# Optimization experiments

Hardware: AMD Instinct MI355X
Metric: run time of the kernel (lower is better)

Reference implementation:

```python
import jax, jax.numpy as jnp
import numpy as np

N = 50000   # nodes in both graphs
E = 800000  # edges per graph
IN = 128
OUT = 64
NEG_SLOPE = 0.2  # DGL GATConv default


def setup_inputs() -> dict:
    key = jax.random.key(0)
    ks = jax.random.split(key, 12)
    stdv = 1.0 / np.sqrt(OUT)
    return {
        'h': jax.random.normal(ks[0], (N, IN), dtype=jnp.float32),
        'src0': jax.random.randint(ks[1], (E,), 0, N, dtype=jnp.int32),
        'dst0': jax.random.randint(ks[2], (E,), 0, N, dtype=jnp.int32),
        'row2': jax.random.randint(ks[3], (E,), 0, N, dtype=jnp.int32),
        'col2': jax.random.randint(ks[4], (E,), 0, N, dtype=jnp.int32),
        'adj_val': jax.random.uniform(ks[5], (E,), dtype=jnp.float32),
        # GATConv params (1 head)
        'W_gat': jax.random.normal(ks[6], (IN, OUT), dtype=jnp.float32) * 0.1,
        'attn_l': jax.random.normal(ks[7], (OUT,), dtype=jnp.float32) * 0.1,
        'attn_r': jax.random.normal(ks[8], (OUT,), dtype=jnp.float32) * 0.1,
        'bias_gat': jnp.zeros((OUT,), dtype=jnp.float32),
        # GraphConvolution params
        'W_gc': jax.random.uniform(ks[9], (IN, OUT), minval=-stdv, maxval=stdv, dtype=jnp.float32),
        'bias_gc': jax.random.uniform(ks[10], (OUT,), minval=-stdv, maxval=stdv, dtype=jnp.float32),
    }


def reference(h, src0, dst0, row2, col2, adj_val, W_gat, attn_l, attn_r, bias_gat, W_gc, bias_gc):
    n = h.shape[0]
    # ---- branch 0: GATConv(1 head) + elu activation ----
    feat = h @ W_gat                        # [N, OUT]
    el = feat @ attn_l                      # [N]
    er = feat @ attn_r                      # [N]
    e = el[src0] + er[dst0]                 # [E]
    e = jnp.where(e > 0, e, NEG_SLOPE * e)  # leaky_relu
    # edge softmax over incoming edges of each dst (stable)
    m = jax.ops.segment_max(e, dst0, num_segments=n)
    ex = jnp.exp(e - m[dst0])
    s = jax.ops.segment_sum(ex, dst0, num_segments=n)
    alpha = ex / s[dst0]                    # [E]
    agg = jax.ops.segment_sum(alpha[:, None] * feat[src0], dst0, num_segments=n)
    z1 = jax.nn.elu(agg + bias_gat)         # [N, OUT]
    # ---- branch 1: GraphConvolution: elu(adj @ (h @ W) + b) ----
    support = h @ W_gc                      # [N, OUT]
    gc = jax.ops.segment_sum(adj_val[:, None] * support[col2], row2, num_segments=n)
    z2 = jax.nn.elu(gc + bias_gc)           # [N, OUT]
    # ---- semantic attention tail (forward is just split+concat) ----
    return jnp.concatenate((z1, z2), axis=1)  # [N, 2*OUT]
```

## Files before the change

kernel.cpp:

```cpp
#include <hip/hip_runtime.h>
#include <hip/hip_bf16.h>
#include <math.h>

#define IN_F 128
#define OUT_F 64
#define BKT_SH 8
#define BKT_MASK 255
#define CHUNK 4096
#define MAXTB 800
#define IDX_BITS 24
#define IDX_MASK ((1u << IDX_BITS) - 1u)
#define PAD 16

typedef __attribute__((ext_vector_type(8))) short bf16x8;
typedef __attribute__((ext_vector_type(4))) float f32x4;

__device__ inline short f2bf(float x) {
    __hip_bfloat16 b = __float2bfloat16(x);
    return *reinterpret_cast<short*>(&b);
}
__device__ inline float bflo(unsigned u) { return __uint_as_float(u << 16); }
__device__ inline float bfhi(unsigned u) { return __uint_as_float(u & 0xffff0000u); }

__global__ __launch_bounds__(256) void k_fused(const float* __restrict__ h,
                                               const float* __restrict__ Wg,
                                               const float* __restrict__ Wc,
                                               const float* __restrict__ attn_l,
                                               const float* __restrict__ attn_r,
                                               __hip_bfloat16* __restrict__ feat,
                                               __hip_bfloat16* __restrict__ support,
                                               float* __restrict__ el,
                                               float* __restrict__ er, int n, int G1,
                                               const int* __restrict__ dst0,
                                               const int* __restrict__ row2,
                                               int* __restrict__ bcnt,
                                               int* __restrict__ chunkhist,
                                               int NB, int E_) {
    __shared__ short Wl[16][128][8];
    __shared__ int hist[MAXTB];

    if ((int)blockIdx.x >= G1) {
        int TB = 2 * NB;
        int t = threadIdx.x;
        int chunk = (int)blockIdx.x - G1;
        for (int i = t; i < TB; i += 256) hist[i] = 0;
        __syncthreads();
        int e0 = chunk * CHUNK;
        for (int i = t; i < CHUNK; i += 256) {
            int e = e0 + i;
            if (e < E_) {
                atomicAdd(&hist[dst0[e] >> BKT_SH], 1);
                atomicAdd(&hist[NB + (row2[e] >> BKT_SH)], 1);
            }
        }
        __syncthreads();
        int* hrow = chunkhist + (size_t)chunk * TB;
        for (int b = t; b < TB; b += 256) {
            int c = hist[b];
            hrow[b] = c;
            if (c) atomicAdd(&bcnt[b * PAD], c);
        }
        return;
    }

    for (int i = threadIdx.x; i < 128 * 32; i += 256) {
        int k = i >> 5;
        int c4 = (i & 31) << 2;
        float4 v4 = (c4 < 64) ? *(const float4*)(Wg + k * 64 + c4)
                              : *(const float4*)(Wc + k * 64 + (c4 - 64));
        short* dst = &Wl[k >> 3][c4][k & 7];
        dst[0]  = f2bf(v4.x);
        dst[8]  = f2bf(v4.y);
        dst[16] = f2bf(v4.z);
        dst[24] = f2bf(v4.w);
    }
    __syncthreads();

    int lane = threadIdx.x & 63;
    int wv = threadIdx.x >> 6;
    int li = lane & 15, lg = lane >> 4;
    int row0 = blockIdx.x * 64 + wv * 16;

    f32x4 acc[8];
#pragma unroll
    for (int ct = 0; ct < 8; ++ct) acc[ct] = (f32x4){0.f, 0.f, 0.f, 0.f};

    int ar = row0 + li;
    if (ar >= n) ar = n - 1;
    const float* hrow = h + (size_t)ar * IN_F + lg * 8;
#pragma unroll
    for (int q = 0; q < 4; ++q) {
        float4 a0 = *(const float4*)(hrow + q * 32);
        float4 a1 = *(const float4*)(hrow + q * 32 + 4);
        bf16x8 af;
        af[0] = f2bf(a0.x); af[1] = f2bf(a0.y); af[2] = f2bf(a0.z); af[3] = f2bf(a0.w);
        af[4] = f2bf(a1.x); af[5] = f2bf(a1.y); af[6] = f2bf(a1.z); af[7] = f2bf(a1.w);
        int kg = q * 4 + lg;
#pragma unroll
        for (int ct = 0; ct < 8; ++ct) {
            bf16x8 bfr = *(const bf16x8*)&Wl[kg][ct * 16 + li][0];
            acc[ct] = __builtin_amdgcn_mfma_f32_16x16x32_bf16(af, bfr, acc[ct], 0, 0, 0);
        }
    }

    float alv[4], arv[4];
#pragma unroll
    for (int ct = 0; ct < 4; ++ct) {
        alv[ct] = attn_l[ct * 16 + li];
        arv[ct] = attn_r[ct * 16 + li];
    }
#pragma unroll
    for (int r = 0; r < 4; ++r) {
        int row = row0 + lg * 4 + r;
        float pl = 0.f, pr = 0.f;
#pragma unroll
        for (int ct = 0; ct < 4; ++ct) {
            pl += acc[ct][r] * alv[ct];
            pr += acc[ct][r] * arv[ct];
        }
#pragma unroll
        for (int m = 8; m; m >>= 1) {
            pl += __shfl_xor(pl, m);
            pr += __shfl_xor(pr, m);
        }
        if (li == 0 && row < n) { el[row] = pl; er[row] = pr; }
    }

#pragma unroll
    for (int r = 0; r < 4; ++r) {
        int row = row0 + lg * 4 + r;
        if (row >= n) continue;
#pragma unroll
        for (int ct = 0; ct < 4; ++ct)
            feat[(size_t)row * OUT_F + ct * 16 + li] = __float2bfloat16(acc[ct][r]);
#pragma unroll
        for (int ct = 4; ct < 8; ++ct)
            support[(size_t)row * OUT_F + (ct - 4) * 16 + li] = __float2bfloat16(acc[ct][r]);
    }
}

__global__ __launch_bounds__(256) void k_part(const int* __restrict__ src0,
                                              const int* __restrict__ dst0,
                                              const int* __restrict__ row2,
                                              const int* __restrict__ col2,
                                              const float* __restrict__ adj_val,
                                              const float* __restrict__ el,
                                              const float* __restrict__ er,
                                              const int* __restrict__ bcnt,
                                              const int* __restrict__ chunkhist,
                                              int* __restrict__ gfill,
                                              int* __restrict__ boffs,
                                              int* __restrict__ offs, int tot,
                                              int2* __restrict__ tmp,
                                              int NB, int E_, int grand) {
    __shared__ int bo[MAXTB + 1];
    __shared__ int hist[MAXTB];
    __shared__ int rbase[MAXTB];
    __shared__ int sh[256];
    int TB = 2 * NB;
    int t = threadIdx.x;

    {
        int base = t * 4;
        int v[4];
        int sum = 0;
#pragma unroll
        for (int i = 0; i < 4; ++i) {
            int idx = base + i;
            v[i] = (idx < TB) ? bcnt[idx * PAD] : 0;
            sum += v[i];
        }
        sh[t] = sum;
        __syncthreads();
        for (int off = 1; off < 256; off <<= 1) {
            int x = (t >= off) ? sh[t - off] : 0;
            __syncthreads();
            sh[t] += x;
            __syncthreads();
        }
        int run = sh[t] - sum;
#pragma unroll
        for (int i = 0; i < 4; ++i) {
            int idx = base + i;
            if (idx < TB) bo[idx] = run;
            run += v[i];
        }
        if (t == 0) bo[TB] = grand;
    }
    __syncthreads();

    if (blockIdx.x == 0) {
        for (int b = t; b <= TB; b += 256) boffs[b] = bo[b];
        if (t == 0) offs[tot] = grand;
    }

    const int* hrow = chunkhist + (size_t)blockIdx.x * TB;
    for (int b = t; b < TB; b += 256) {
        int c = hrow[b];
        int bb = 0;
        if (c) bb = bo[b] + atomicAdd(&gfill[b * PAD], c);
        rbase[b] = bb;
        hist[b] = 0;
    }
    __syncthreads();
    int e0 = blockIdx.x * CHUNK;
    for (int i = t; i < CHUNK; i += 256) {
        int e = e0 + i;
        if (e < E_) {
            int s = src0[e];
            int d = dst0[e];
            int b = d >> BKT_SH;
            int p = atomicAdd(&hist[b], 1);
            float w = el[s] + er[d];
            w = w > 0.f ? w : 0.2f * w;
            w = __expf(w);
            tmp[(size_t)rbase[b] + p] =
                make_int2((int)(((unsigned)(d & BKT_MASK) << IDX_BITS) | (unsigned)s),
                          __float_as_int(w));
            int r = row2[e];
            int b2 = NB + (r >> BKT_SH);
            int p2 = atomicAdd(&hist[b2], 1);
            tmp[(size_t)rbase[b2] + p2] =
                make_int2((int)(((unsigned)(r & BKT_MASK) << IDX_BITS) | (unsigned)col2[e]),
                          __float_as_int(adj_val[e]));
        }
    }
}

__global__ __launch_bounds__(256) void k_bbuild(const int2* __restrict__ tmp,
                                                const int* __restrict__ boffs,
                                                int* __restrict__ offs,
                                                int2* __restrict__ ew, int NB, int n) {
    __shared__ int hcnt[256], hoff[256], hfill[256], sh[256];
    int b = blockIdx.x;
    int t = threadIdx.x;
    int base = boffs[b];
    int cnt = boffs[b + 1] - base;
    bool isGat = b < NB;
    int nodeBase = (isGat ? b : b - NB) << BKT_SH;
    int offsBase = (isGat ? 0 : n) + nodeBase;

    hcnt[t] = 0;
    hfill[t] = 0;
    __syncthreads();
    for (int i = t; i < cnt; i += 256)
        atomicAdd(&hcnt[((unsigned)tmp[(size_t)base + i].x) >> IDX_BITS], 1);
    __syncthreads();
    sh[t] = hcnt[t];
    __syncthreads();
    for (int off = 1; off < 256; off <<= 1) {
        int x = (t >= off) ? sh[t - off] : 0;
        __syncthreads();
        sh[t] += x;
        __syncthreads();
    }
    hoff[t] = sh[t] - hcnt[t];
    if (nodeBase + t < n) offs[offsBase + t] = base + hoff[t];
    __syncthreads();
    for (int i = t; i < cnt; i += 256) {
        int2 v = tmp[(size_t)base + i];
        unsigned loc = ((unsigned)v.x) >> IDX_BITS;
        int p = atomicAdd(&hfill[loc], 1);
        ew[(size_t)base + hoff[loc] + p] =
            make_int2((int)((unsigned)v.x & IDX_MASK), v.y);
    }
}

__global__ __launch_bounds__(256) void k_agg(const int2* __restrict__ ew,
                                             const int* __restrict__ offs,
                                             const __hip_bfloat16* __restrict__ feat,
                                             const __hip_bfloat16* __restrict__ support,
                                             const float* __restrict__ bias_gat,
                                             const float* __restrict__ bias_gc,
                                             float* __restrict__ out, int n) {
    int wave = (int)(((long long)blockIdx.x * blockDim.x + threadIdx.x) >> 6);
    int lane = threadIdx.x & 63;
    int nq = (n + 3) >> 2;
    if (wave >= 2 * nq) return;
    int q = lane >> 4;
    int fg = lane & 15;
    int qb = q << 4;

    bool isGat = wave < nq;
    int node = (isGat ? wave : wave - nq) * 4 + q;
    bool nodeValid = node < n;
    int wid = (isGat ? 0 : n) + (nodeValid ? node : 0);
    int start = offs[wid];
    int deg = nodeValid ? offs[wid + 1] - start : 0;

    const uint2* fbase = (const uint2*)(isGat ? feat : support);
    float acc[4] = {0.f, 0.f, 0.f, 0.f};
    float sw = 0.f;

    for (int c0 = 0; c0 < deg; c0 += 16) {
        int cnt = min(16, deg - c0);
        bool valid = fg < cnt;
        int2 e = valid ? ew[(size_t)start + c0 + fg] : make_int2(0, 0);
        float w = __int_as_float(e.y);
        float ts = w;
        ts += __shfl_xor(ts, 1);  ts += __shfl_xor(ts, 2);
        ts += __shfl_xor(ts, 4);  ts += __shfl_xor(ts, 8);
        sw += ts;
#pragma unroll 4
        for (int k = 0; k < cnt; ++k) {
            float wk = __shfl(w, qb + k);
            int ik = __shfl(e.x, qb + k);
            uint2 pv = fbase[(size_t)ik * 16 + fg];
            acc[0] += wk * bflo(pv.x); acc[1] += wk * bfhi(pv.x);
            acc[2] += wk * bflo(pv.y); acc[3] += wk * bfhi(pv.y);
        }
    }
    if (nodeValid) {
        float inv = isGat ? (deg > 0 ? __builtin_amdgcn_rcpf(sw) : 0.f) : 1.f;
        const float* bias = isGat ? bias_gat : bias_gc;
        int outoff = isGat ? 0 : OUT_F;
        float4 bb = *(const float4*)(bias + fg * 4);
        float z0 = acc[0] * inv + bb.x;
        float z1 = acc[1] * inv + bb.y;
        float z2 = acc[2] * inv + bb.z;
        float z3 = acc[3] * inv + bb.w;
        z0 = z0 > 0.f ? z0 : __expf(z0) - 1.f;
        z1 = z1 > 0.f ? z1 : __expf(z1) - 1.f;
        z2 = z2 > 0.f ? z2 : __expf(z2) - 1.f;
        z3 = z3 > 0.f ? z3 : __expf(z3) - 1.f;
        *(float4*)(out + (size_t)node * 128 + outoff + fg * 4) = make_float4(z0, z1, z2, z3);
    }
}

extern "C" void kernel_launch(void* const* d_in, const int* in_sizes, int n_in,
                              void* d_out, int out_size, void* d_ws, size_t ws_size,
                              hipStream_t stream) {
    const float* h        = (const float*)d_in[0];
    const int*   src0     = (const int*)d_in[1];
    const int*   dst0     = (const int*)d_in[2];
    const int*   row2     = (const int*)d_in[3];
    const int*   col2     = (const int*)d_in[4];
    const float* adj_val  = (const float*)d_in[5];
    const float* Wg       = (const float*)d_in[6];
    const float* attn_l   = (const float*)d_in[7];
    const float* attn_r   = (const float*)d_in[8];
    const float* bias_gat = (const float*)d_in[9];
    const float* Wc       = (const float*)d_in[10];
    const float* bias_gc  = (const float*)d_in[11];

    int n  = in_sizes[0] / IN_F;
    int E_ = in_sizes[1];
    float* out = (float*)d_out;

    int NB = (n + BKT_MASK) >> BKT_SH;
    int TB = 2 * NB;
    if (TB > MAXTB) return;
    if (n >= (1 << IDX_BITS) || E_ >= (1 << IDX_BITS)) return;

    int nchunk = (E_ + CHUNK - 1) / CHUNK;

    char* p = (char*)d_ws;
    auto alloc = [&](size_t bytes, size_t align) -> void* {
        size_t a = ((size_t)p + align - 1) & ~(align - 1);
        p = (char*)(a + bytes);
        return (void*)a;
    };
    size_t Rbytes = 2 * (size_t)E_ * sizeof(int2);
    if ((size_t)nchunk * TB * sizeof(int) > Rbytes) return;
    char* R = (char*)alloc(Rbytes, 256);
    int*  chunkhist = (int*)R;
    int2* ew        = (int2*)R;
    int2*  tmp   = (int2*) alloc(2 * (size_t)E_ * sizeof(int2), 256);
    int*   offs  = (int*)  alloc((2 * (size_t)n + 1) * sizeof(int), 16);
    float* el    = (float*)alloc((size_t)n * sizeof(float), 16);
    float* er    = (float*)alloc((size_t)n * sizeof(float), 16);
    int*   bcnt  = (int*)  alloc(2 * (size_t)TB * PAD * sizeof(int), 64);
    int*   gfill = bcnt + TB * PAD;
    int*   boffs = (int*)  alloc(((size_t)TB + 1) * sizeof(int), 16);
    __hip_bfloat16* feat    = (__hip_bfloat16*)alloc((size_t)n * OUT_F * sizeof(__hip_bfloat16), 256);
    __hip_bfloat16* support = (__hip_bfloat16*)alloc((size_t)n * OUT_F * sizeof(__hip_bfloat16), 256);
    size_t need = (size_t)(p - (char*)d_ws);
    if (ws_size < need) return;

    int G1 = (n + 63) / 64;

    hipMemsetAsync(bcnt, 0, 2 * (size_t)TB * PAD * sizeof(int), stream);
    k_fused<<<G1 + nchunk, 256, 0, stream>>>(h, Wg, Wc, attn_l, attn_r,
                                             feat, support, el, er, n, G1,
                                             dst0, row2, bcnt, chunkhist, NB, E_);
    k_part<<<nchunk, 256, 0, stream>>>(src0, dst0, row2, col2, adj_val,
                                       el, er, bcnt, chunkhist, gfill,
                                       boffs, offs, 2 * n, tmp, NB, E_, 2 * E_);
    k_bbuild<<<TB, 256, 0, stream>>>(tmp, boffs, offs, ew, NB, n);
    int nq = (n + 3) >> 2;
    long long aggthreads = 2LL * nq * 64;
    k_agg<<<(int)((aggthreads + 255) / 256), 256, 0, stream>>>(
        ew, offs, feat, support, bias_gat, bias_gc, out, n);
}
```

Measured before the change: 121.0 us.

## Pack edge entries to 32-bit bf16 weight plus 16-bit index; split aggregation per branch

```diff
diff --git a/kernel.cpp b/kernel.cpp
--- a/kernel.cpp
+++ b/kernel.cpp
@@ -230,7 +230,7 @@
 __global__ __launch_bounds__(256) void k_bbuild(const int2* __restrict__ tmp,
                                                 const int* __restrict__ boffs,
                                                 int* __restrict__ offs,
-                                                int2* __restrict__ ew, int NB, int n) {
+                                                unsigned* __restrict__ ew, int NB, int n) {
     __shared__ int hcnt[256], hoff[256], hfill[256], sh[256];
     int b = blockIdx.x;
     int t = threadIdx.x;
@@ -261,59 +261,57 @@
         int2 v = tmp[(size_t)base + i];
         unsigned loc = ((unsigned)v.x) >> IDX_BITS;
         int p = atomicAdd(&hfill[loc], 1);
-        ew[(size_t)base + hoff[loc] + p] =
-            make_int2((int)((unsigned)v.x & IDX_MASK), v.y);
-    }
-}
-
-__global__ __launch_bounds__(256) void k_agg(const int2* __restrict__ ew,
+        unsigned idx16 = ((unsigned)v.x & IDX_MASK) & 0xffffu;
+        unsigned wbits = (unsigned)(unsigned short)f2bf(__int_as_float(v.y));
+        ew[(size_t)base + hoff[loc] + p] = (wbits << 16) | idx16;
+    }
+}
+
+__global__ __launch_bounds__(256) void k_agg(const unsigned* __restrict__ ew,
                                              const int* __restrict__ offs,
-                                             const __hip_bfloat16* __restrict__ feat,
-                                             const __hip_bfloat16* __restrict__ support,
-                                             const float* __restrict__ bias_gat,
-                                             const float* __restrict__ bias_gc,
-                                             float* __restrict__ out, int n) {
+                                             const __hip_bfloat16* __restrict__ fb,
+                                             const float* __restrict__ bias,
+                                             float* __restrict__ out, int n,
+                                             int offsBase, int outoff, int norm) {
     int wave = (int)(((long long)blockIdx.x * blockDim.x + threadIdx.x) >> 6);
     int lane = threadIdx.x & 63;
     int nq = (n + 3) >> 2;
-    if (wave >= 2 * nq) return;
+    if (wave >= nq) return;
     int q = lane >> 4;
     int fg = lane & 15;
     int qb = q << 4;
 
-    bool isGat = wave < nq;
-    int node = (isGat ? wave : wave - nq) * 4 + q;
+    int node = wave * 4 + q;
     bool nodeValid = node < n;
-    int wid = (isGat ? 0 : n) + (nodeValid ? node : 0);
+    int wid = offsBase + (nodeValid ? node : 0);
     int start = offs[wid];
     int deg = nodeValid ? offs[wid + 1] - start : 0;
 
-    const uint2* fbase = (const uint2*)(isGat ? feat : support);
+    const uint2* fbase = (const uint2*)fb;
     float acc[4] = {0.f, 0.f, 0.f, 0.f};
     float sw = 0.f;
 
     for (int c0 = 0; c0 < deg; c0 += 16) {
         int cnt = min(16, deg - c0);
         bool valid = fg < cnt;
-        int2 e = valid ? ew[(size_t)start + c0 + fg] : make_int2(0, 0);
-        float w = __int_as_float(e.y);
+        unsigned e = valid ? ew[(size_t)start + c0 + fg] : 0u;
+        float w = bfhi(e);
         float ts = w;
         ts += __shfl_xor(ts, 1);  ts += __shfl_xor(ts, 2);
         ts += __shfl_xor(ts, 4);  ts += __shfl_xor(ts, 8);
         sw += ts;
 #pragma unroll 4
         for (int k = 0; k < cnt; ++k) {
-            float wk = __shfl(w, qb + k);
-            int ik = __shfl(e.x, qb + k);
+            unsigned ek = (unsigned)__shfl((int)e, qb + k);
+            float wk = bfhi(ek);
+            int ik = (int)(ek & 0xffffu);
             uint2 pv = fbase[(size_t)ik * 16 + fg];
             acc[0] += wk * bflo(pv.x); acc[1] += wk * bfhi(pv.x);
             acc[2] += wk * bflo(pv.y); acc[3] += wk * bfhi(pv.y);
         }
     }
     if (nodeValid) {
-        float inv = isGat ? (deg > 0 ? __builtin_amdgcn_rcpf(sw) : 0.f) : 1.f;
-        const float* bias = isGat ? bias_gat : bias_gc;
-        int outoff = isGat ? 0 : OUT_F;
+        float inv = norm ? (deg > 0 ? __builtin_amdgcn_rcpf(sw) : 0.f) : 1.f;
         float4 bb = *(const float4*)(bias + fg * 4);
         float z0 = acc[0] * inv + bb.x;
         float z1 = acc[1] * inv + bb.y;
@@ -350,7 +348,8 @@
     int NB = (n + BKT_MASK) >> BKT_SH;
     int TB = 2 * NB;
     if (TB > MAXTB) return;
-    if (n >= (1 << IDX_BITS) || E_ >= (1 << IDX_BITS)) return;
+    if (n > 65536) return;
+    if (E_ >= (1 << IDX_BITS)) return;
 
     int nchunk = (E_ + CHUNK - 1) / CHUNK;
 
@@ -363,8 +362,8 @@
     size_t Rbytes = 2 * (size_t)E_ * sizeof(int2);
     if ((size_t)nchunk * TB * sizeof(int) > Rbytes) return;
     char* R = (char*)alloc(Rbytes, 256);
-    int*  chunkhist = (int*)R;
-    int2* ew        = (int2*)R;
+    int*      chunkhist = (int*)R;
+    unsigned* ew        = (unsigned*)R;
     int2*  tmp   = (int2*) alloc(2 * (size_t)E_ * sizeof(int2), 256);
     int*   offs  = (int*)  alloc((2 * (size_t)n + 1) * sizeof(int), 16);
     float* el    = (float*)alloc((size_t)n * sizeof(float), 16);
@@ -388,7 +387,9 @@
                                        boffs, offs, 2 * n, tmp, NB, E_, 2 * E_);
     k_bbuild<<<TB, 256, 0, stream>>>(tmp, boffs, offs, ew, NB, n);
     int nq = (n + 3) >> 2;
-    long long aggthreads = 2LL * nq * 64;
-    k_agg<<<(int)((aggthreads + 255) / 256), 256, 0, stream>>>(
-        ew, offs, feat, support, bias_gat, bias_gc, out, n);
-}
+    int aggblocks = (int)(((long long)nq * 64 + 255) / 256);
+    k_agg<<<aggblocks, 256, 0, stream>>>(ew, offs, feat, bias_gat, out, n,
+                                         0, 0, 1);
+    k_agg<<<aggblocks, 256, 0, stream>>>(ew, offs, support, bias_gc, out, n,
+                                         n, OUT_F, 0);
+}
```

Result: slower. 125.3 us (+3.6%).

## Pack CSR edges into 32-bit bf16 weight plus 16-bit index; widen partition blocks

Applied to the files above, without the earlier changes.

```diff
diff --git a/kernel.cpp b/kernel.cpp
--- a/kernel.cpp
+++ b/kernel.cpp
@@ -139,63 +139,49 @@
     }
 }
 
-__global__ __launch_bounds__(256) void k_part(const int* __restrict__ src0,
-                                              const int* __restrict__ dst0,
-                                              const int* __restrict__ row2,
-                                              const int* __restrict__ col2,
-                                              const float* __restrict__ adj_val,
-                                              const float* __restrict__ el,
-                                              const float* __restrict__ er,
-                                              const int* __restrict__ bcnt,
-                                              const int* __restrict__ chunkhist,
-                                              int* __restrict__ gfill,
-                                              int* __restrict__ boffs,
-                                              int* __restrict__ offs, int tot,
-                                              int2* __restrict__ tmp,
-                                              int NB, int E_, int grand) {
+__global__ __launch_bounds__(1024) void k_part(const int* __restrict__ src0,
+                                               const int* __restrict__ dst0,
+                                               const int* __restrict__ row2,
+                                               const int* __restrict__ col2,
+                                               const float* __restrict__ adj_val,
+                                               const float* __restrict__ el,
+                                               const float* __restrict__ er,
+                                               const int* __restrict__ bcnt,
+                                               const int* __restrict__ chunkhist,
+                                               int* __restrict__ gfill,
+                                               int* __restrict__ boffs,
+                                               int* __restrict__ offs, int tot,
+                                               int2* __restrict__ tmp,
+                                               int NB, int E_, int grand) {
     __shared__ int bo[MAXTB + 1];
     __shared__ int hist[MAXTB];
     __shared__ int rbase[MAXTB];
-    __shared__ int sh[256];
+    __shared__ int sh[1024];
     int TB = 2 * NB;
     int t = threadIdx.x;
 
     {
-        int base = t * 4;
-        int v[4];
-        int sum = 0;
-#pragma unroll
-        for (int i = 0; i < 4; ++i) {
-            int idx = base + i;
-            v[i] = (idx < TB) ? bcnt[idx * PAD] : 0;
-            sum += v[i];
-        }
-        sh[t] = sum;
-        __syncthreads();
-        for (int off = 1; off < 256; off <<= 1) {
+        int v = (t < TB) ? bcnt[t * PAD] : 0;
+        sh[t] = v;
+        __syncthreads();
+        for (int off = 1; off < 1024; off <<= 1) {
             int x = (t >= off) ? sh[t - off] : 0;
             __syncthreads();
             sh[t] += x;
             __syncthreads();
         }
-        int run = sh[t] - sum;
-#pragma unroll
-        for (int i = 0; i < 4; ++i) {
-            int idx = base + i;
-            if (idx < TB) bo[idx] = run;
-            run += v[i];
-        }
+        if (t < TB) bo[t] = sh[t] - v;
         if (t == 0) bo[TB] = grand;
     }
     __syncthreads();
 
     if (blockIdx.x == 0) {
-        for (int b = t; b <= TB; b += 256) boffs[b] = bo[b];
+        for (int b = t; b <= TB; b += 1024) boffs[b] = bo[b];
         if (t == 0) offs[tot] = grand;
     }
 
     const int* hrow = chunkhist + (size_t)blockIdx.x * TB;
-    for (int b = t; b < TB; b += 256) {
+    for (int b = t; b < TB; b += 1024) {
         int c = hrow[b];
         int bb = 0;
         if (c) bb = bo[b] + atomicAdd(&gfill[b * PAD], c);
@@ -204,7 +190,7 @@
     }
     __syncthreads();
     int e0 = blockIdx.x * CHUNK;
-    for (int i = t; i < CHUNK; i += 256) {
+    for (int i = t; i < CHUNK; i += 1024) {
         int e = e0 + i;
         if (e < E_) {
             int s = src0[e];
@@ -230,7 +216,7 @@
 __global__ __launch_bounds__(256) void k_bbuild(const int2* __restrict__ tmp,
                                                 const int* __restrict__ boffs,
                                                 int* __restrict__ offs,
-                                                int2* __restrict__ ew, int NB, int n) {
+                                                unsigned* __restrict__ ew, int NB, int n) {
     __shared__ int hcnt[256], hoff[256], hfill[256], sh[256];
     int b = blockIdx.x;
     int t = threadIdx.x;
@@ -261,12 +247,13 @@
         int2 v = tmp[(size_t)base + i];
         unsigned loc = ((unsigned)v.x) >> IDX_BITS;
         int p = atomicAdd(&hfill[loc], 1);
-        ew[(size_t)base + hoff[loc] + p] =
-            make_int2((int)((unsigned)v.x & IDX_MASK), v.y);
-    }
-}
-
-__global__ __launch_bounds__(256) void k_agg(const int2* __restrict__ ew,
+        unsigned idx16 = ((unsigned)v.x & IDX_MASK) & 0xffffu;
+        unsigned wbits = (unsigned)(unsigned short)f2bf(__int_as_float(v.y));
+        ew[(size_t)base + hoff[loc] + p] = (wbits << 16) | idx16;
+    }
+}
+
+__global__ __launch_bounds__(256) void k_agg(const unsigned* __restrict__ ew,
                                              const int* __restrict__ offs,
                                              const __hip_bfloat16* __restrict__ feat,
                                              const __hip_bfloat16* __restrict__ support,
@@ -295,16 +282,17 @@
     for (int c0 = 0; c0 < deg; c0 += 16) {
         int cnt = min(16, deg - c0);
         bool valid = fg < cnt;
-        int2 e = valid ? ew[(size_t)start + c0 + fg] : make_int2(0, 0);
-        float w = __int_as_float(e.y);
+        unsigned e = valid ? ew[(size_t)start + c0 + fg] : 0u;
+        float w = bfhi(e);
         float ts = w;
         ts += __shfl_xor(ts, 1);  ts += __shfl_xor(ts, 2);
         ts += __shfl_xor(ts, 4);  ts += __shfl_xor(ts, 8);
         sw += ts;
 #pragma unroll 4
         for (int k = 0; k < cnt; ++k) {
-            float wk = __shfl(w, qb + k);
-            int ik = __shfl(e.x, qb + k);
+            unsigned ek = (unsigned)__shfl((int)e, qb + k);
+            float wk = bfhi(ek);
+            int ik = (int)(ek & 0xffffu);
             uint2 pv = fbase[(size_t)ik * 16 + fg];
             acc[0] += wk * bflo(pv.x); acc[1] += wk * bfhi(pv.x);
             acc[2] += wk * bflo(pv.y); acc[3] += wk * bfhi(pv.y);
@@ -350,7 +338,8 @@
     int NB = (n + BKT_MASK) >> BKT_SH;
     int TB = 2 * NB;
     if (TB > MAXTB) return;
-    if (n >= (1 << IDX_BITS) || E_ >= (1 << IDX_BITS)) return;
+    if (n > 65536) return;
+    if (E_ >= (1 << IDX_BITS)) return;
 
     int nchunk = (E_ + CHUNK - 1) / CHUNK;
 
@@ -363,8 +352,8 @@
     size_t Rbytes = 2 * (size_t)E_ * sizeof(int2);
     if ((size_t)nchunk * TB * sizeof(int) > Rbytes) return;
     char* R = (char*)alloc(Rbytes, 256);
-    int*  chunkhist = (int*)R;
-    int2* ew        = (int2*)R;
+    int*      chunkhist = (int*)R;
+    unsigned* ew        = (unsigned*)R;
     int2*  tmp   = (int2*) alloc(2 * (size_t)E_ * sizeof(int2), 256);
     int*   offs  = (int*)  alloc((2 * (size_t)n + 1) * sizeof(int), 16);
     float* el    = (float*)alloc((size_t)n * sizeof(float), 16);
@@ -383,9 +372,9 @@
     k_fused<<<G1 + nchunk, 256, 0, stream>>>(h, Wg, Wc, attn_l, attn_r,
                                              feat, support, el, er, n, G1,
                                              dst0, row2, bcnt, chunkhist, NB, E_);
-    k_part<<<nchunk, 256, 0, stream>>>(src0, dst0, row2, col2, adj_val,
-                                       el, er, bcnt, chunkhist, gfill,
-                                       boffs, offs, 2 * n, tmp, NB, E_, 2 * E_);
+    k_part<<<nchunk, 1024, 0, stream>>>(src0, dst0, row2, col2, adj_val,
+                                        el, er, bcnt, chunkhist, gfill,
+                                        boffs, offs, 2 * n, tmp, NB, E_, 2 * E_);
     k_bbuild<<<TB, 256, 0, stream>>>(tmp, boffs, offs, ew, NB, n);
     int nq = (n + 3) >> 2;
     long long aggthreads = 2LL * nq * 64;
```

Result: faster. 117.0 us, median of 2 (-3.3%).
